# Kernel optimization log

Measured on AMD Instinct MI355X. Metric: run time of the kernel, lower is better.

## Reference

```python
import jax, jax.numpy as jnp
import numpy as np

D_MODEL = 1024
N_HEADS = 16
D_K = D_MODEL // N_HEADS  # 64
SCALE = 0.125             # attention_scale = 1/sqrt(d_k)
ROPE_BASE = 10000.0
NEG_INF = -1e30


def setup_inputs() -> dict:
    key = jax.random.key(0)
    k1, k2, k3 = jax.random.split(key, 3)
    B, S = 2, 2048
    x = jax.random.normal(k1, (B, S, D_MODEL), jnp.float32)
    # torch Linear(d_model, 3*d_model, bias=False): stored here as [in, out]
    w_qkv = jax.random.normal(k2, (D_MODEL, 3 * D_MODEL), jnp.float32) * (D_MODEL ** -0.5)
    w_o = jax.random.normal(k3, (D_MODEL, D_MODEL), jnp.float32) * (D_MODEL ** -0.5)
    return {"x": x, "w_qkv": w_qkv, "w_o": w_o}


def _rotary(x):
    # x: [B, H, S, D]; standard half-split rotary over sequence positions
    S, D = x.shape[2], x.shape[3]
    inv_freq = 1.0 / (ROPE_BASE ** (jnp.arange(0, D, 2, dtype=jnp.float32) / D))  # [D/2]
    freqs = jnp.arange(S, dtype=jnp.float32)[:, None] * inv_freq[None, :]          # [S, D/2]
    cos = jnp.cos(freqs)[None, None]  # [1,1,S,D/2]
    sin = jnp.sin(freqs)[None, None]
    x1, x2 = jnp.split(x, 2, axis=-1)
    return jnp.concatenate([x1 * cos + x2 * sin, -x1 * sin + x2 * cos], axis=-1).astype(x.dtype)


def reference(x, w_qkv, w_o):
    B, S, _ = x.shape
    qkv = x @ w_qkv                                        # [B,S,3*D_MODEL]
    qkv = qkv.reshape(B, S, 3, N_HEADS, D_K).transpose(2, 0, 3, 1, 4)  # [3,B,H,S,Dk]
    q, k, v = qkv[0], qkv[1], qkv[2]
    q = _rotary(q)
    k = _rotary(k)
    scores = jnp.einsum('bhqd,bhkd->bhqk', q, k) * SCALE   # [B,H,S,S]
    causal = jnp.tril(jnp.ones((S, S), dtype=bool))
    scores = jnp.where(causal, scores, NEG_INF)
    attn = jax.nn.softmax(scores, axis=-1)
    out = jnp.einsum('bhqk,bhkd->bhqd', attn, v)           # [B,H,S,Dk]
    out = out.transpose(0, 2, 1, 3).reshape(B, S, D_MODEL)
    return out @ w_o
```

## Files before the change

### kernel.cpp

```cpp
#include <hip/hip_runtime.h>

typedef short bf16x8 __attribute__((ext_vector_type(8)));
typedef short bf16x4 __attribute__((ext_vector_type(4)));
typedef float f32x4 __attribute__((ext_vector_type(4)));
typedef float f32x16 __attribute__((ext_vector_type(16)));
typedef int i32x4 __attribute__((ext_vector_type(4)));

#define DEVI static __device__ __forceinline__

DEVI unsigned short f2b(float f) {
  unsigned u = __float_as_uint(f);
  u += 0x7FFFu + ((u >> 16) & 1u);
  return (unsigned short)(u >> 16);
}

DEVI void gload16(const void* g, void* l) {
  __builtin_amdgcn_global_load_lds((const __attribute__((address_space(1))) void*)g,
                                   (__attribute__((address_space(3))) void*)l, 16, 0, 0);
}

DEVI void pl32swap(int a, int b, int& outa, int& outb) {
#if __has_builtin(__builtin_amdgcn_permlane32_swap)
  auto r = __builtin_amdgcn_permlane32_swap(a, b, false, false);
  outa = ((const int*)&r)[0];
  outb = ((const int*)&r)[1];
#else
  int bp = __shfl_xor(b, 32);
  int ap = __shfl_xor(a, 32);
  outa = (threadIdx.x & 32) ? bp : a;
  outb = (threadIdx.x & 32) ? b : ap;
#endif
}

DEVI float halfmax(float x) {
  int o0, o1;
  pl32swap(__float_as_int(x), __float_as_int(x), o0, o1);
  return fmaxf(__int_as_float(o0), __int_as_float(o1));
}
DEVI float halfsum(float x) {
  int o0, o1;
  pl32swap(__float_as_int(x), __float_as_int(x), o0, o1);
  return __int_as_float(o0) + __int_as_float(o1);
}

__global__ void rope_table_kernel(float* __restrict__ ct, float* __restrict__ st) {
  int i = blockIdx.x * 256 + threadIdx.x;
  int s = i >> 5, j = i & 31;
  float inv = powf(10000.0f, -(float)j * (1.0f / 32.0f));
  float a = (float)s * inv;
  ct[i] = cosf(a);
  st[i] = sinf(a);
}

__global__ void cvt_x_kernel(const float* __restrict__ x, unsigned short* __restrict__ xb) {
  int i = blockIdx.x * 256 + threadIdx.x;
  float4 v = ((const float4*)x)[i];
  ushort4 o;
  o.x = f2b(v.x); o.y = f2b(v.y); o.z = f2b(v.z); o.w = f2b(v.w);
  ((ushort4*)xb)[i] = o;
}

__global__ void transpose_kernel(const float* __restrict__ W, unsigned short* __restrict__ WT,
                                 int K, int N) {
  __shared__ float tile[32][33];
  int n0 = blockIdx.x * 32, k0 = blockIdx.y * 32;
  int tx = threadIdx.x, ty = threadIdx.y;
#pragma unroll
  for (int i = 0; i < 32; i += 8)
    tile[ty + i][tx] = W[(size_t)(k0 + ty + i) * N + n0 + tx];
  __syncthreads();
#pragma unroll
  for (int i = 0; i < 32; i += 8)
    WT[(size_t)(n0 + ty + i) * K + k0 + tx] = f2b(tile[tx][ty + i]);
}

__global__ __launch_bounds__(512, 2) void gemm_qkv_kernel(
    const unsigned short* __restrict__ Xb, const unsigned short* __restrict__ WT,
    const float* __restrict__ ct, const float* __restrict__ st,
    unsigned short* __restrict__ Qb, unsigned short* __restrict__ Kb,
    unsigned short* __restrict__ VTb) {
  __shared__ unsigned short As[2][256 * 64];
  __shared__ unsigned short Bs[2][256 * 64];
  const int tid = threadIdx.x;
  const int lane = tid & 63, wid = tid >> 6;
  const int m0 = blockIdx.y * 256, n0 = blockIdx.x * 256;
  const int wr = wid >> 2, wc = wid & 3;
  const int srow = lane >> 3;
  const int scc = ((lane & 7) ^ srow) * 8;
  const int rx = lane & 7;

  f32x4 acc[8][4] = {};

  auto stage = [&](int k0, int nb) {
    unsigned short* Ad = As[nb];
    unsigned short* Bd = Bs[nb];
#pragma unroll
    for (int i = 0; i < 4; ++i) {
      const int c = i * 8 + wid;
      const int row = c * 8 + srow;
      gload16(Xb + (size_t)(m0 + row) * 1024 + k0 + scc, (char*)Ad + c * 1024);
      gload16(WT + (size_t)(n0 + row) * 1024 + k0 + scc, (char*)Bd + c * 1024);
    }
  };
  auto compute = [&](int nb) {
    const unsigned short* Ab = As[nb];
    const unsigned short* Bb = Bs[nb];
#pragma unroll
    for (int kk = 0; kk < 64; kk += 32) {
      const int cc = (((kk >> 3) + (lane >> 4)) ^ rx) * 8;
      bf16x8 a[8], b[4];
#pragma unroll
      for (int mi = 0; mi < 8; ++mi)
        a[mi] = *(const bf16x8*)&Ab[(wr * 128 + mi * 16 + (lane & 15)) * 64 + cc];
#pragma unroll
      for (int ni = 0; ni < 4; ++ni)
        b[ni] = *(const bf16x8*)&Bb[(wc * 64 + ni * 16 + (lane & 15)) * 64 + cc];
      __builtin_amdgcn_s_setprio(1);
#pragma unroll
      for (int mi = 0; mi < 8; ++mi)
#pragma unroll
        for (int ni = 0; ni < 4; ++ni)
          acc[mi][ni] = __builtin_amdgcn_mfma_f32_16x16x32_bf16(a[mi], b[ni], acc[mi][ni], 0, 0, 0);
      __builtin_amdgcn_s_setprio(0);
    }
  };

  stage(0, 0);
  stage(64, 1);
  for (int t = 0; t < 15; ++t) {
    asm volatile("s_waitcnt vmcnt(8)" ::: "memory");
    __builtin_amdgcn_s_barrier();
    compute(t & 1);
    __builtin_amdgcn_s_barrier();
    if (t < 14) stage((t + 2) * 64, t & 1);
  }
  asm volatile("s_waitcnt vmcnt(0)" ::: "memory");
  __builtin_amdgcn_s_barrier();
  compute(1);

  const int n_base = n0 + wc * 64;
  const int ty = n_base >> 10;
  const int h = (n_base & 1023) >> 6;
  if (ty < 2) {
    unsigned short* dst = (ty == 0) ? Qb : Kb;
#pragma unroll
    for (int mi = 0; mi < 8; ++mi) {
      const int mrow = m0 + wr * 128 + mi * 16 + ((lane >> 4) << 2);
#pragma unroll
      for (int r = 0; r < 4; ++r) {
        const int m = mrow + r;
        const int s = m & 2047, bb = m >> 11;
        const size_t base = ((size_t)(bb * 16 + h) * 2048 + s) * 64;
#pragma unroll
        for (int ni = 0; ni < 2; ++ni) {
          const int j = ni * 16 + (lane & 15);
          const float c = ct[s * 32 + j], sn = st[s * 32 + j];
          const float x1 = acc[mi][ni][r], x2 = acc[mi][ni + 2][r];
          dst[base + j]      = f2b(x1 * c + x2 * sn);
          dst[base + j + 32] = f2b(-x1 * sn + x2 * c);
        }
      }
    }
  } else {
#pragma unroll
    for (int mi = 0; mi < 8; ++mi) {
      const int mrow = m0 + wr * 128 + mi * 16 + ((lane >> 4) << 2);
      const int s = mrow & 2047, bb = mrow >> 11;
#pragma unroll
      for (int ni = 0; ni < 4; ++ni) {
        const int d = ni * 16 + (lane & 15);
        ushort4 o;
        o.x = f2b(acc[mi][ni][0]); o.y = f2b(acc[mi][ni][1]);
        o.z = f2b(acc[mi][ni][2]); o.w = f2b(acc[mi][ni][3]);
        *(ushort4*)&VTb[((size_t)(bb * 16 + h) * 64 + d) * 2048 + s] = o;
      }
    }
  }
}

DEVI void gemm_mainloop(const unsigned short* __restrict__ A, const unsigned short* __restrict__ B,
                        unsigned short* As, unsigned short* Bs,
                        int m0, int n0, int lane, int wid, int wr, int wc,
                        f32x4 acc[4][4]) {
  const int srow = lane >> 3;
  const int scc = ((lane & 7) ^ srow) * 8;
  const int rx = lane & 7;
  auto stage = [&](int k0, int nb) {
    unsigned short* Ad = As + nb * 8192;
    unsigned short* Bd = Bs + nb * 8192;
#pragma unroll
    for (int i = 0; i < 4; ++i) {
      const int c = i * 4 + wid;
      const int row = c * 8 + srow;
      gload16(A + (size_t)(m0 + row) * 1024 + k0 + scc, (char*)Ad + c * 1024);
      gload16(B + (size_t)(n0 + row) * 1024 + k0 + scc, (char*)Bd + c * 1024);
    }
  };
  auto compute = [&](int nb) {
    const unsigned short* Ab = As + nb * 8192;
    const unsigned short* Bb = Bs + nb * 8192;
#pragma unroll
    for (int kk = 0; kk < 64; kk += 32) {
      const int cc = (((kk >> 3) + (lane >> 4)) ^ rx) * 8;
      bf16x8 a[4], b[4];
#pragma unroll
      for (int mi = 0; mi < 4; ++mi)
        a[mi] = *(const bf16x8*)&Ab[(wr * 64 + mi * 16 + (lane & 15)) * 64 + cc];
#pragma unroll
      for (int ni = 0; ni < 4; ++ni)
        b[ni] = *(const bf16x8*)&Bb[(wc * 64 + ni * 16 + (lane & 15)) * 64 + cc];
      __builtin_amdgcn_s_setprio(1);
#pragma unroll
      for (int mi = 0; mi < 4; ++mi)
#pragma unroll
        for (int ni = 0; ni < 4; ++ni)
          acc[mi][ni] = __builtin_amdgcn_mfma_f32_16x16x32_bf16(a[mi], b[ni], acc[mi][ni], 0, 0, 0);
      __builtin_amdgcn_s_setprio(0);
    }
  };
  stage(0, 0);
  stage(64, 1);
  for (int t = 0; t < 15; ++t) {
    asm volatile("s_waitcnt vmcnt(8)" ::: "memory");
    __builtin_amdgcn_s_barrier();
    compute(t & 1);
    __builtin_amdgcn_s_barrier();
    if (t < 14) stage((t + 2) * 64, t & 1);
  }
  asm volatile("s_waitcnt vmcnt(0)" ::: "memory");
  __builtin_amdgcn_s_barrier();
  compute(1);
}

DEVI void stage128(const unsigned short* __restrict__ Kh, const unsigned short* __restrict__ Vh,
                   int kbase, unsigned char* buf , int tid) {
  const int r = tid >> 3, c = tid & 7, cc = c ^ (r & 7);
  const int dst = (tid & ~63) * 16;
#pragma unroll
  for (int q = 0; q < 2; ++q) {
    unsigned char* b = buf + q * 16384;
    gload16(Kh + (size_t)(kbase + q * 64 + r) * 64 + cc * 8, b + dst);
    gload16(Vh + (size_t)r * 2048 + kbase + q * 64 + cc * 8, b + 8192 + dst);
  }
}

DEVI void attn_sub(const unsigned char* __restrict__ bufK, const unsigned char* __restrict__ bufV,
                   const bf16x8 qf[4], int s32, int kglob, bool diag, int qg, int ln, int hi,
                   float& m2, float& l_run, f32x16& acc0, f32x16& acc1) {
  const float C = 0.125f * 1.44269504f;
  const int rx = ln & 7;
  bf16x8 kf[4];
#pragma unroll
  for (int j = 0; j < 4; ++j) {
    const int cc = (2 * j + hi) ^ rx;
    kf[j] = *(const bf16x8*)(bufK + (s32 * 32 + ln) * 128 + cc * 16);
  }
  bf16x8 v0[2], v1[2];
#pragma unroll
  for (int p = 0; p < 2; ++p) {
    const int cc = (4 * s32 + 2 * p + hi) ^ rx;
    v0[p] = *(const bf16x8*)(bufV + ln * 128 + cc * 16);
    v1[p] = *(const bf16x8*)(bufV + (ln + 32) * 128 + cc * 16);
  }

  f32x16 stv = {};
  __builtin_amdgcn_s_setprio(1);
  stv = __builtin_amdgcn_mfma_f32_32x32x16_bf16(kf[0], qf[0], stv, 0, 0, 0);
  stv = __builtin_amdgcn_mfma_f32_32x32x16_bf16(kf[1], qf[1], stv, 0, 0, 0);
  stv = __builtin_amdgcn_mfma_f32_32x32x16_bf16(kf[2], qf[2], stv, 0, 0, 0);
  stv = __builtin_amdgcn_mfma_f32_32x32x16_bf16(kf[3], qf[3], stv, 0, 0, 0);
  __builtin_amdgcn_s_setprio(0);

  float sraw[16];
#pragma unroll
  for (int r = 0; r < 16; ++r) sraw[r] = stv[r];
  if (diag) {
#pragma unroll
    for (int r = 0; r < 16; ++r) {
      const int kg = kglob + (r & 3) + ((r >> 2) << 3) + (hi << 2);
      if (kg > qg) sraw[r] = -1e30f;
    }
  }
  float mraw = sraw[0];
#pragma unroll
  for (int r = 1; r < 16; ++r) mraw = fmaxf(mraw, sraw[r]);
  const float mloc = halfmax(mraw * C);
  if (__any(mloc > m2 + 11.5416f)) {
    const float mnew = fmaxf(m2, mloc);
    const float sc = exp2f(m2 - mnew);
    l_run *= sc;
#pragma unroll
    for (int r = 0; r < 16; ++r) { acc0[r] *= sc; acc1[r] *= sc; }
    m2 = mnew;
  }
  float p[16], ps = 0.f;
#pragma unroll
  for (int r = 0; r < 16; ++r) { p[r] = exp2f(fmaf(sraw[r], C, -m2)); ps += p[r]; }
  l_run += halfsum(ps);

  int cw[8];
#pragma unroll
  for (int i = 0; i < 8; ++i)
    asm("v_cvt_pk_bf16_f32 %0, %1, %2" : "=v"(cw[i]) : "v"(p[2 * i]), "v"(p[2 * i + 1]));
  int a0, a1, b0, b1, a2, a3, b2, b3;
  pl32swap(cw[0], cw[2], a0, b0);
  pl32swap(cw[1], cw[3], a1, b1);
  pl32swap(cw[4], cw[6], a2, b2);
  pl32swap(cw[5], cw[7], a3, b3);
  const bf16x8 pa0 = __builtin_bit_cast(bf16x8, (i32x4){a0, a1, b0, b1});
  const bf16x8 pa1 = __builtin_bit_cast(bf16x8, (i32x4){a2, a3, b2, b3});

  __builtin_amdgcn_s_setprio(1);
  acc0 = __builtin_amdgcn_mfma_f32_32x32x16_bf16(v0[0], pa0, acc0, 0, 0, 0);
  acc0 = __builtin_amdgcn_mfma_f32_32x32x16_bf16(v0[1], pa1, acc0, 0, 0, 0);
  acc1 = __builtin_amdgcn_mfma_f32_32x32x16_bf16(v1[0], pa0, acc1, 0, 0, 0);
  acc1 = __builtin_amdgcn_mfma_f32_32x32x16_bf16(v1[1], pa1, acc1, 0, 0, 0);
  __builtin_amdgcn_s_setprio(0);
}

DEVI void write_partial(float* M, int slot, const f32x16& a0, const f32x16& a1,
                        float m2, float l) {
#pragma unroll
  for (int r = 0; r < 16; ++r) { M[slot + r] = a0[r]; M[slot + 16 + r] = a1[r]; }
  M[slot + 32] = m2;
  M[slot + 33] = l;
}

DEVI void write_merged(unsigned short* __restrict__ Ob, const float* M, int slot,
                       const f32x16& acc0, const f32x16& acc1, float m2, float l_run,
                       int bh, int q0, int ln, int hi) {
  const float mp = M[slot + 32], lp = M[slot + 33];
  const float m = fmaxf(m2, mp);
  const float eo = exp2f(m2 - m), ep = exp2f(mp - m);
  const float il = 1.0f / (l_run * eo + lp * ep);
  const int b = bh >> 4, h = bh & 15;
  unsigned short* ob = Ob + ((size_t)(b * 2048 + q0 + ln)) * 1024 + h * 64;
#pragma unroll
  for (int g = 0; g < 4; ++g) {
    ushort4 o0, o1;
    o0.x = f2b((acc0[4 * g + 0] * eo + M[slot + 4 * g + 0] * ep) * il);
    o0.y = f2b((acc0[4 * g + 1] * eo + M[slot + 4 * g + 1] * ep) * il);
    o0.z = f2b((acc0[4 * g + 2] * eo + M[slot + 4 * g + 2] * ep) * il);
    o0.w = f2b((acc0[4 * g + 3] * eo + M[slot + 4 * g + 3] * ep) * il);
    o1.x = f2b((acc1[4 * g + 0] * eo + M[slot + 16 + 4 * g + 0] * ep) * il);
    o1.y = f2b((acc1[4 * g + 1] * eo + M[slot + 16 + 4 * g + 1] * ep) * il);
    o1.z = f2b((acc1[4 * g + 2] * eo + M[slot + 16 + 4 * g + 2] * ep) * il);
    o1.w = f2b((acc1[4 * g + 3] * eo + M[slot + 16 + 4 * g + 3] * ep) * il);
    *(ushort4*)&ob[8 * g + 4 * hi]      = o0;
    *(ushort4*)&ob[32 + 8 * g + 4 * hi] = o1;
  }
}

__global__ __launch_bounds__(512) void attn_kernel(
    const unsigned short* __restrict__ Qb, const unsigned short* __restrict__ Kb,
    const unsigned short* __restrict__ VTb, unsigned short* __restrict__ Ob) {
  __shared__ unsigned char smem[2][2][16384];
  const int tid = threadIdx.x;
  const int lane = tid & 63, wid = tid >> 6;
  const int ln = lane & 31, hi = lane >> 5;
  const int s = wid & 3, half = wid >> 2;
  const int bh = blockIdx.x;
  const int p = blockIdx.y;
  const int jA = 15 - p, jB = p;
  const unsigned short* Qh = Qb + (size_t)bh * 2048 * 64;
  const unsigned short* Kh = Kb + (size_t)bh * 2048 * 64;
  const unsigned short* Vh = VTb + (size_t)bh * 64 * 2048;

  f32x16 aA0 = {}, aA1 = {}, aB0 = {}, aB1 = {};
  float mA = -1e30f, lA = 0.f, mB = -1e30f, lB = 0.f;
  int it = 0;

  auto load_q = [&](int q0, bf16x8 qf[4]) {
    const unsigned short* pq = Qh + (size_t)(q0 + ln) * 64 + hi * 8;
#pragma unroll
    for (int t = 0; t < 4; ++t) qf[t] = *(const bf16x8*)(pq + t * 16);
  };
  auto run_phase = [&](int j, const bf16x8 qf[4], f32x16& acc0, f32x16& acc1,
                       float& m2, float& l_run, int q0, int nextFirst) {
    const int qg = q0 + ln;
    const int top = q0 >> 5;
    for (int kb = 0; kb <= j; ++kb, ++it) {
      const int nxt = (kb < j) ? (kb + 1) * 128 : nextFirst;
      if (nxt >= 0) stage128(Kh, Vh, nxt, &smem[(it + 1) & 1][0][0], tid);
      const unsigned char* bufK = &smem[it & 1][half][0];
      const unsigned char* bufV = bufK + 8192;
      const int t64 = 2 * kb + half;
#pragma unroll
      for (int s32 = 0; s32 < 2; ++s32) {
        const int g32 = 2 * t64 + s32;
        if (g32 <= top)
          attn_sub(bufK, bufV, qf, s32, g32 * 32, g32 == top, qg, ln, hi, m2, l_run, acc0, acc1);
      }
      __syncthreads();
    }
  };

  bf16x8 qfA[4];
  load_q(jA * 128 + s * 32, qfA);
  stage128(Kh, Vh, 0, &smem[0][0][0], tid);
  __syncthreads();
  run_phase(jA, qfA, aA0, aA1, mA, lA, jA * 128 + s * 32, 0);
  bf16x8 qfB[4];
  load_q(jB * 128 + s * 32, qfB);
  run_phase(jB, qfB, aB0, aB1, mB, lB, jB * 128 + s * 32, -1);

  float* M = (float*)&smem[0][0][0];
  const int slot = (s * 64 + lane) * 34;
  if (half == 1) write_partial(M, slot, aA0, aA1, mA, lA);
  __syncthreads();
  if (half == 0) write_merged(Ob, M, slot, aA0, aA1, mA, lA, bh, jA * 128 + s * 32, ln, hi);
  __syncthreads();
  if (half == 0) write_partial(M, slot, aB0, aB1, mB, lB);
  __syncthreads();
  if (half == 1) write_merged(Ob, M, slot, aB0, aB1, mB, lB, bh, jB * 128 + s * 32, ln, hi);
}

__global__ __launch_bounds__(256) void gemm_out_kernel(
    const unsigned short* __restrict__ Ob, const unsigned short* __restrict__ WoT,
    float* __restrict__ out) {
  __shared__ unsigned short As[2][128 * 64];
  __shared__ unsigned short Bs[2][128 * 64];
  const int lane = threadIdx.x & 63, wid = threadIdx.x >> 6;
  const int m0 = blockIdx.y * 128, n0 = blockIdx.x * 128;
  const int wr = wid >> 1, wc = wid & 1;
  f32x4 acc[4][4] = {};
  gemm_mainloop(Ob, WoT, &As[0][0], &Bs[0][0], m0, n0, lane, wid, wr, wc, acc);
#pragma unroll
  for (int mi = 0; mi < 4; ++mi) {
    const int mrow = m0 + wr * 64 + mi * 16 + ((lane >> 4) << 2);
#pragma unroll
    for (int ni = 0; ni < 4; ++ni) {
      const int n = n0 + wc * 64 + ni * 16 + (lane & 15);
#pragma unroll
      for (int r = 0; r < 4; ++r)
        out[(size_t)(mrow + r) * 1024 + n] = acc[mi][ni][r];
    }
  }
}

extern "C" void kernel_launch(void* const* d_in, const int* in_sizes, int n_in,
                              void* d_out, int out_size, void* d_ws, size_t ws_size,
                              hipStream_t stream) {
  const float* x     = (const float*)d_in[0];
  const float* w_qkv = (const float*)d_in[1];
  const float* w_o   = (const float*)d_in[2];
  float* out = (float*)d_out;
  char* ws = (char*)d_ws;

  const size_t MB = 1 << 20;
  float* ct = (float*)(ws);
  float* st = (float*)(ws + (256 << 10));
  unsigned short* Xb  = (unsigned short*)(ws + (512 << 10));
  unsigned short* WqT = (unsigned short*)(ws + (512 << 10) + 8  * MB);
  unsigned short* WoT = (unsigned short*)(ws + (512 << 10) + 14 * MB);
  unsigned short* Qb  = (unsigned short*)(ws + (512 << 10) + 16 * MB);
  unsigned short* Kb  = (unsigned short*)(ws + (512 << 10) + 24 * MB);
  unsigned short* VTb = (unsigned short*)(ws + (512 << 10) + 32 * MB);
  unsigned short* Ob  = Xb;

  rope_table_kernel<<<dim3(256), dim3(256), 0, stream>>>(ct, st);
  cvt_x_kernel<<<dim3(4096), dim3(256), 0, stream>>>(x, Xb);
  transpose_kernel<<<dim3(96, 32), dim3(32, 8), 0, stream>>>(w_qkv, WqT, 1024, 3072);
  transpose_kernel<<<dim3(32, 32), dim3(32, 8), 0, stream>>>(w_o, WoT, 1024, 1024);
  gemm_qkv_kernel<<<dim3(12, 16), dim3(512), 0, stream>>>(Xb, WqT, ct, st, Qb, Kb, VTb);
  attn_kernel<<<dim3(32, 8), dim3(512), 0, stream>>>(Qb, Kb, VTb, Ob);
  gemm_out_kernel<<<dim3(8, 32), dim3(256), 0, stream>>>(Ob, WoT, out);
}
```

Baseline: 123.5 us.

## Interleave QKV GEMM global loads with MFMA quads and remap blocks for L2 locality

The QKV projection GEMM main loop is restructured. Each K-step is split into four MFMA quads, and the global-to-LDS loads for future tiles are issued between them, with finer barriers and vmcnt waits, so memory traffic overlaps compute instead of sitting in one burst. A block index remap also groups workgroups by a stride of 8 (likely matching XCD dispatch) so tiles sharing X or W rows run together and get better cache reuse. The cost is more barriers per iteration and more complex hazard reasoning around partially staged buffers.

New measurement: 124.3 us. About the same (+0.7%).

```diff
diff --git a/kernel.cpp b/kernel.cpp
--- a/kernel.cpp
+++ b/kernel.cpp
@@ -83,7 +83,10 @@
   __shared__ unsigned short Bs[2][256 * 64];
   const int tid = threadIdx.x;
   const int lane = tid & 63, wid = tid >> 6;
-  const int m0 = blockIdx.y * 256, n0 = blockIdx.x * 256;
+  const int flat = blockIdx.y * 12 + blockIdx.x;
+  const int nf = (flat & 7) * 24 + (flat >> 3);
+  const int bx = nf % 12, by = nf / 12;
+  const int m0 = by * 256, n0 = bx * 256;
   const int wr = wid >> 2, wc = wid & 3;
   const int srow = lane >> 3;
   const int scc = ((lane & 7) ^ srow) * 8;
@@ -91,52 +94,93 @@
 
   f32x4 acc[8][4] = {};
 
-  auto stage = [&](int k0, int nb) {
-    unsigned short* Ad = As[nb];
-    unsigned short* Bd = Bs[nb];
-#pragma unroll
-    for (int i = 0; i < 4; ++i) {
-      const int c = i * 8 + wid;
-      const int row = c * 8 + srow;
-      gload16(Xb + (size_t)(m0 + row) * 1024 + k0 + scc, (char*)Ad + c * 1024);
-      gload16(WT + (size_t)(n0 + row) * 1024 + k0 + scc, (char*)Bd + c * 1024);
-    }
-  };
-  auto compute = [&](int nb) {
-    const unsigned short* Ab = As[nb];
-    const unsigned short* Bb = Bs[nb];
-#pragma unroll
-    for (int kk = 0; kk < 64; kk += 32) {
-      const int cc = (((kk >> 3) + (lane >> 4)) ^ rx) * 8;
-      bf16x8 a[8], b[4];
-#pragma unroll
-      for (int mi = 0; mi < 8; ++mi)
-        a[mi] = *(const bf16x8*)&Ab[(wr * 128 + mi * 16 + (lane & 15)) * 64 + cc];
+  auto stageA = [&](int k0, int nb, int i) {
+    const int c = i * 8 + wid;
+    const int row = c * 8 + srow;
+    gload16(Xb + (size_t)(m0 + row) * 1024 + k0 + scc, (char*)As[nb] + c * 1024);
+  };
+  auto stageB = [&](int k0, int nb, int i) {
+    const int c = i * 8 + wid;
+    const int row = c * 8 + srow;
+    gload16(WT + (size_t)(n0 + row) * 1024 + k0 + scc, (char*)Bs[nb] + c * 1024);
+  };
+  auto loadA = [&](const unsigned short* Ab, int q, bf16x8 af[2][2]) {
+#pragma unroll
+    for (int kk = 0; kk < 2; ++kk) {
+      const int cc = ((kk * 4 + (lane >> 4)) ^ rx) * 8;
+#pragma unroll
+      for (int miL = 0; miL < 2; ++miL)
+        af[miL][kk] = *(const bf16x8*)&Ab[(wr * 128 + (q * 2 + miL) * 16 + (lane & 15)) * 64 + cc];
+    }
+  };
+
+#define QKV_MFMA_QUAD(Q)                                                      \
+  __builtin_amdgcn_s_barrier();                                               \
+  asm volatile("s_waitcnt lgkmcnt(0)" ::: "memory");                          \
+  __builtin_amdgcn_s_setprio(1);                                              \
+  _Pragma("unroll") for (int kk = 0; kk < 2; ++kk)                            \
+    _Pragma("unroll") for (int miL = 0; miL < 2; ++miL)                       \
+      _Pragma("unroll") for (int ni = 0; ni < 4; ++ni)                        \
+        acc[(Q) * 2 + miL][ni] = __builtin_amdgcn_mfma_f32_16x16x32_bf16(     \
+            af[miL][kk], bf[ni][kk], acc[(Q) * 2 + miL][ni], 0, 0, 0);        \
+  __builtin_amdgcn_s_setprio(0);                                              \
+  __builtin_amdgcn_s_barrier();
+
+#pragma unroll
+  for (int i = 0; i < 4; ++i) stageB(0, 0, i);
+#pragma unroll
+  for (int i = 0; i < 4; ++i) stageA(0, 0, i);
+#pragma unroll
+  for (int i = 0; i < 4; ++i) stageB(64, 1, i);
+  stageA(64, 1, 0); stageA(64, 1, 2);
+  asm volatile("s_waitcnt vmcnt(6)" ::: "memory");
+  __builtin_amdgcn_s_barrier();
+
+  for (int t = 0; t < 16; ++t) {
+    const int b = t & 1;
+    const unsigned short* Ab = As[b];
+    const unsigned short* Bb = Bs[b];
+    const int k1 = (t + 1) * 64, k2 = (t + 2) * 64;
+    bf16x8 bf[4][2], af[2][2];
+
+#pragma unroll
+    for (int kk = 0; kk < 2; ++kk) {
+      const int cc = ((kk * 4 + (lane >> 4)) ^ rx) * 8;
 #pragma unroll
       for (int ni = 0; ni < 4; ++ni)
-        b[ni] = *(const bf16x8*)&Bb[(wc * 64 + ni * 16 + (lane & 15)) * 64 + cc];
-      __builtin_amdgcn_s_setprio(1);
-#pragma unroll
-      for (int mi = 0; mi < 8; ++mi)
+        bf[ni][kk] = *(const bf16x8*)&Bb[(wc * 64 + ni * 16 + (lane & 15)) * 64 + cc];
+    }
+    loadA(Ab, 0, af);
+    if (t + 1 < 16) { stageA(k1, b ^ 1, 1); stageA(k1, b ^ 1, 3); }
+    QKV_MFMA_QUAD(0)
+
+    loadA(Ab, 1, af);
+    if (t + 2 < 16) { stageB(k2, b, 0); stageB(k2, b, 1); }
+    QKV_MFMA_QUAD(1)
+
+    loadA(Ab, 2, af);
+    if (t + 2 < 16) { stageB(k2, b, 2); stageB(k2, b, 3); }
+    QKV_MFMA_QUAD(2)
+
+    loadA(Ab, 3, af);
+    if (t + 2 < 16) { stageA(k2, b, 0); stageA(k2, b, 2); }
+    __builtin_amdgcn_s_barrier();
+    asm volatile("s_waitcnt lgkmcnt(0)" ::: "memory");
+    __builtin_amdgcn_s_setprio(1);
+#pragma unroll
+    for (int kk = 0; kk < 2; ++kk)
+#pragma unroll
+      for (int miL = 0; miL < 2; ++miL)
 #pragma unroll
         for (int ni = 0; ni < 4; ++ni)
-          acc[mi][ni] = __builtin_amdgcn_mfma_f32_16x16x32_bf16(a[mi], b[ni], acc[mi][ni], 0, 0, 0);
-      __builtin_amdgcn_s_setprio(0);
-    }
-  };
-
-  stage(0, 0);
-  stage(64, 1);
-  for (int t = 0; t < 15; ++t) {
-    asm volatile("s_waitcnt vmcnt(8)" ::: "memory");
+          acc[6 + miL][ni] = __builtin_amdgcn_mfma_f32_16x16x32_bf16(
+              af[miL][kk], bf[ni][kk], acc[6 + miL][ni], 0, 0, 0);
+    __builtin_amdgcn_s_setprio(0);
+    if (t + 2 < 16) asm volatile("s_waitcnt vmcnt(6)" ::: "memory");
+    else            asm volatile("s_waitcnt vmcnt(0)" ::: "memory");
     __builtin_amdgcn_s_barrier();
-    compute(t & 1);
-    __builtin_amdgcn_s_barrier();
-    if (t < 14) stage((t + 2) * 64, t & 1);
-  }
-  asm volatile("s_waitcnt vmcnt(0)" ::: "memory");
-  __builtin_amdgcn_s_barrier();
-  compute(1);
+  }
+#undef QKV_MFMA_QUAD
 
   const int n_base = n0 + wc * 64;
   const int ty = n_base >> 10;
```
